# Kernel tuning notes

Measured on AMD Instinct MI355X. Metric: run time of the kernel, lower is better.

The kernel has to match this reference:

```python
import jax, jax.numpy as jnp
import numpy as np

B, T, K = 1024, 512, 64
START, STOP = K - 2, K - 1
NEG = -10000.0


def setup_inputs() -> dict:
    key = jax.random.key(0)
    k1, k2, k3, k4 = jax.random.split(key, 4)
    feats = jax.random.normal(k1, (B, T, K), dtype=jnp.float32)
    lengths = jax.random.randint(k2, (B,), 1, T + 1)  # valid seq lengths in [1, T]
    tags = jax.random.randint(k3, (B, T), 0, K)
    transitions = jax.random.normal(k4, (K, K), dtype=jnp.float32)
    # CRF constraints: nothing transitions INTO start, nothing transitions OUT of stop
    transitions = transitions.at[START, :].set(NEG).at[:, STOP].set(NEG)
    return {"feats": feats, "lengths": lengths, "tags": tags, "transitions": transitions}


def _forward_alg(feats, transitions, lengths):
    Bn, Tn, Kn = feats.shape
    alpha0 = jnp.full((Bn, Kn), NEG, feats.dtype).at[:, START].set(0.0)

    def step(alpha, emit):  # alpha: [B,K] over prev tag j; emit: [B,K] over cur tag i
        # tag_var[b,i,j] = emit[b,i] + trans[i,j] + alpha[b,j]
        new = jax.nn.logsumexp(emit[:, :, None] + transitions[None, :, :] + alpha[:, None, :], axis=2)
        return new, new

    _, ys = jax.lax.scan(step, alpha0, jnp.swapaxes(feats, 0, 1))  # ys: [T,B,K]
    all_alpha = jnp.concatenate([alpha0[None], ys], axis=0)  # [T+1,B,K]
    sel = all_alpha[lengths, jnp.arange(Bn)]  # alpha after `lengths` steps: [B,K]
    terminal = sel + transitions[STOP][None, :]
    return jax.nn.logsumexp(terminal, axis=1)  # [B]


def _score_sentence(feats, transitions, lengths, tags):
    Bn, Tn, Kn = feats.shape
    pad_start = jnp.concatenate([jnp.full((Bn, 1), START, tags.dtype), tags], axis=1)  # [B,T+1]
    pad_stop = jnp.concatenate([tags, jnp.full((Bn, 1), STOP, tags.dtype)], axis=1)  # [B,T+1]
    pos = jnp.arange(Tn + 1)[None, :]
    pad_stop = jnp.where(pos >= lengths[:, None], STOP, pad_stop)  # tags[lengths:] -> STOP
    trans_vals = transitions[pad_stop, pad_start]  # [B,T+1]
    trans_score = jnp.sum(jnp.where(pos <= lengths[:, None], trans_vals, 0.0), axis=1)
    emit_vals = jnp.take_along_axis(feats, tags[:, :, None], axis=2)[:, :, 0]  # [B,T]
    emit_mask = jnp.arange(Tn)[None, :] < lengths[:, None]
    emit_score = jnp.sum(jnp.where(emit_mask, emit_vals, 0.0), axis=1)
    return trans_score + emit_score


def reference(feats, lengths, tags, transitions):
    forward_score = _forward_alg(feats, transitions, lengths)
    gold_score = _score_sentence(feats, transitions, lengths, tags)
    return jnp.mean(forward_score - gold_score)
```

## Files before the change

kernel.cpp:

```cpp
#include <hip/hip_runtime.h>

#define CRF_B 1024
#define CRF_T 512
#define CRF_K 64
#define CRF_START 62
#define CRF_STOP 63

typedef float vf16 __attribute__((ext_vector_type(16)));

__device__ __forceinline__ float bcastf(float v, int lane) {
  return __int_as_float(__builtin_amdgcn_readlane(__float_as_int(v), lane));
}

__device__ __forceinline__ float wave_max64(float v) {
#pragma unroll
  for (int off = 32; off > 0; off >>= 1) v = fmaxf(v, __shfl_xor(v, off, 64));
  return v;
}

__device__ __forceinline__ float wave_sum64(float v) {
#pragma unroll
  for (int off = 32; off > 0; off >>= 1) v += __shfl_xor(v, off, 64);
  return v;
}

__global__ __launch_bounds__(128, 1) void crf_kernel(
    const float* __restrict__ feats, const int* __restrict__ lengths,
    const int* __restrict__ tags, const float* __restrict__ trans,
    float* __restrict__ out) {
  __shared__ float sT[CRF_K * 65];

  const int b = blockIdx.x;
  const int tid = threadIdx.x;
  const int lane = tid & 63;

  for (int idx = tid; idx < CRF_K * CRF_K; idx += 128)
    sT[(idx >> 6) * 65 + (idx & 63)] = trans[idx];
  __syncthreads();

  const int L = lengths[b];

  if (tid < 64) {
    vf16 E0, E1, E2, E3;
    {
      const float* trow = &sT[lane * 65];
#pragma unroll
      for (int j = 0; j < 16; ++j) E0[j] = __expf(trow[j]);
#pragma unroll
      for (int j = 0; j < 16; ++j) E1[j] = __expf(trow[16 + j]);
#pragma unroll
      for (int j = 0; j < 16; ++j) E2[j] = __expf(trow[32 + j]);
#pragma unroll
      for (int j = 0; j < 16; ++j) E3[j] = __expf(trow[48 + j]);
    }

    const float* bfeats = feats + (size_t)b * CRF_T * CRF_K + lane;

    float P = (lane == CRF_START) ? 1.0f : 0.0f;
    float offset = 0.0f;

    float e[8], f[8];
#pragma unroll
    for (int r = 0; r < 8; ++r) e[r] = bfeats[r * CRF_K];

    auto do_step = [&](float ee) {
      float a0 = 0.f, a1 = 0.f, a2 = 0.f, a3 = 0.f;
#pragma unroll
      for (int j = 0; j < 16; ++j) a0 = __builtin_fmaf(E0[j], bcastf(P, j), a0);
#pragma unroll
      for (int j = 0; j < 16; ++j) a1 = __builtin_fmaf(E1[j], bcastf(P, 16 + j), a1);
#pragma unroll
      for (int j = 0; j < 16; ++j) a2 = __builtin_fmaf(E2[j], bcastf(P, 32 + j), a2);
#pragma unroll
      for (int j = 0; j < 15; ++j) a3 = __builtin_fmaf(E3[j], bcastf(P, 48 + j), a3);
      P = ((a0 + a1) + (a2 + a3)) * ee;
    };

    auto rescale = [&](int first) {
      float M = first ? 1.0f : bcastf(P, 0);
      offset += __logf(M);
      P *= __builtin_amdgcn_rcpf(M);
    };

    const int Lb = L & ~7;
    for (int t0 = 0; t0 < Lb; t0 += 8) {
      const int tn = t0 + 8;
      if (tn < CRF_T) {
#pragma unroll
        for (int r = 0; r < 8; ++r) f[r] = bfeats[(tn + r) * CRF_K];
      } else {
#pragma unroll
        for (int r = 0; r < 8; ++r) f[r] = 0.0f;
      }
      float ee[8];
#pragma unroll
      for (int r = 0; r < 8; ++r) ee[r] = __expf(e[r]);

      rescale(t0 == 0);

#pragma unroll
      for (int r = 0; r < 8; ++r) do_step(ee[r]);
#pragma unroll
      for (int r = 0; r < 8; ++r) e[r] = f[r];
    }

    if (Lb < L) {
      rescale(Lb == 0);
#pragma unroll
      for (int r = 0; r < 8; ++r) {
        if (Lb + r < L) do_step(__expf(e[r]));
      }
    }

    float eST = __expf(sT[CRF_STOP * 65 + lane]);
    float v = P * eST;
    float s2 = wave_sum64(v);
    float fwd = offset + __logf(s2);
    if (lane == 0) atomicAdd(out, fwd * (1.0f / CRF_B));
  } else {
    const int* btags = tags + b * CRF_T;
    const float* bf = feats + (size_t)b * CRF_T * CRF_K;
    float gold = 0.0f;
#pragma unroll
    for (int base = 0; base < CRF_T; base += 64) {
      int t = base + lane;
      if (t < L) {
        int tg = btags[t];
        int tp = (t == 0) ? CRF_START : btags[t - 1];
        gold += bf[(size_t)t * CRF_K + tg];
        gold += sT[tg * 65 + tp];
      }
    }
    gold = wave_sum64(gold);
    if (lane == 0) {
      gold += sT[CRF_STOP * 65 + btags[L - 1]];
      atomicAdd(out, -gold * (1.0f / CRF_B));
    }
  }
}

extern "C" void kernel_launch(void* const* d_in, const int* in_sizes, int n_in,
                              void* d_out, int out_size, void* d_ws, size_t ws_size,
                              hipStream_t stream) {
  const float* feats = (const float*)d_in[0];
  const int* lengths = (const int*)d_in[1];
  const int* tags = (const int*)d_in[2];
  const float* trans = (const float*)d_in[3];
  float* out = (float*)d_out;
  hipMemsetAsync(out, 0, sizeof(float), stream);
  crf_kernel<<<CRF_B, 128, 0, stream>>>(feats, lengths, tags, trans, out);
}
```

Before: 299.7 us.

## Use packed fp16 dot2 for CRF forward recursion with per-step power-of-two rescaling

Each forward step's 64-wide dot product moves from fp32 FMAs with 63 readlane broadcasts to packed fp16 v_dot2 instructions on lane pairs. A DPP pair-swap packs two probabilities per lane, so only 32 readlanes are needed. Rescaling now happens every step, using a DPP wave-max and an exponent shift tracked as an integer offset, replacing the old per-8-step log/rcp rescale. This halves the broadcast and FMA count but adds a per-step max reduction and fp16 precision risk on exp(transitions) values, which can overflow or underflow fp16.

```diff
diff --git a/kernel.cpp b/kernel.cpp
--- a/kernel.cpp
+++ b/kernel.cpp
@@ -6,17 +6,23 @@
 #define CRF_START 62
 #define CRF_STOP 63
 
+typedef _Float16 hh2 __attribute__((ext_vector_type(2)));
+typedef unsigned int vu16 __attribute__((ext_vector_type(16)));
 typedef float vf16 __attribute__((ext_vector_type(16)));
+
+#if __has_builtin(__builtin_amdgcn_fdot2)
+#define USE_DOT2 1
+#else
+#define USE_DOT2 0
+#endif
 
 __device__ __forceinline__ float bcastf(float v, int lane) {
   return __int_as_float(__builtin_amdgcn_readlane(__float_as_int(v), lane));
 }
 
-__device__ __forceinline__ float wave_max64(float v) {
-#pragma unroll
-  for (int off = 32; off > 0; off >>= 1) v = fmaxf(v, __shfl_xor(v, off, 64));
-  return v;
-}
+#define DPP_F(x, ctrl, rmask)                                                 \
+  __int_as_float(__builtin_amdgcn_update_dpp(0, __float_as_int(x), ctrl,      \
+                                             rmask, 0xf, true))
 
 __device__ __forceinline__ float wave_sum64(float v) {
 #pragma unroll
@@ -41,45 +47,91 @@
   const int L = lengths[b];
 
   if (tid < 64) {
+    const float* trow = &sT[lane * 65];
+#if USE_DOT2
+    vu16 EA, EB;
+#pragma unroll
+    for (int jp = 0; jp < 16; ++jp) {
+      hh2 v;
+      v.x = (_Float16)__expf(trow[2 * jp]);
+      v.y = (_Float16)__expf(trow[2 * jp + 1]);
+      EA[jp] = __builtin_bit_cast(unsigned int, v);
+    }
+#pragma unroll
+    for (int jp = 0; jp < 16; ++jp) {
+      hh2 v;
+      v.x = (_Float16)__expf(trow[32 + 2 * jp]);
+      v.y = (_Float16)__expf(trow[32 + 2 * jp + 1]);
+      EB[jp] = __builtin_bit_cast(unsigned int, v);
+    }
+#else
     vf16 E0, E1, E2, E3;
-    {
-      const float* trow = &sT[lane * 65];
 #pragma unroll
-      for (int j = 0; j < 16; ++j) E0[j] = __expf(trow[j]);
+    for (int j = 0; j < 16; ++j) E0[j] = __expf(trow[j]);
 #pragma unroll
-      for (int j = 0; j < 16; ++j) E1[j] = __expf(trow[16 + j]);
+    for (int j = 0; j < 16; ++j) E1[j] = __expf(trow[16 + j]);
 #pragma unroll
-      for (int j = 0; j < 16; ++j) E2[j] = __expf(trow[32 + j]);
+    for (int j = 0; j < 16; ++j) E2[j] = __expf(trow[32 + j]);
 #pragma unroll
-      for (int j = 0; j < 16; ++j) E3[j] = __expf(trow[48 + j]);
-    }
+    for (int j = 0; j < 16; ++j) E3[j] = __expf(trow[48 + j]);
+#endif
 
     const float* bfeats = feats + (size_t)b * CRF_T * CRF_K + lane;
 
     float P = (lane == CRF_START) ? 1.0f : 0.0f;
-    float offset = 0.0f;
+    int offs = 0;
 
     float e[8], f[8];
 #pragma unroll
     for (int r = 0; r < 8; ++r) e[r] = bfeats[r * CRF_K];
 
     auto do_step = [&](float ee) {
+      float m = P;
+      m = fmaxf(m, DPP_F(m, 0x111, 0xf));
+      m = fmaxf(m, DPP_F(m, 0x112, 0xf));
+      m = fmaxf(m, DPP_F(m, 0x114, 0xf));
+      m = fmaxf(m, DPP_F(m, 0x118, 0xf));
+      m = fmaxf(m, DPP_F(m, 0x142, 0xa));
+      m = fmaxf(m, DPP_F(m, 0x143, 0xc));
+      float mx = bcastf(m, 63);
+      int ex = ((__float_as_int(mx) >> 23) & 0xff) - 126;
+      offs += ex;
+      float Pn = P * __int_as_float((127 - ex) << 23);
+#if USE_DOT2
+      _Float16 h = (_Float16)Pn;
+      int hi = (int)(unsigned short)__builtin_bit_cast(unsigned short, h);
+      int hn = __builtin_amdgcn_update_dpp(0, hi, 0xB1, 0xf, 0xf, true);
+      hh2 hp;
+      hp.x = h;
+      hp.y = __builtin_bit_cast(_Float16, (unsigned short)hn);
+      int hpi = __builtin_bit_cast(int, hp);
+      int rl[4];
+#pragma unroll
+      for (int q = 0; q < 4; ++q) rl[q] = __builtin_amdgcn_readlane(hpi, 2 * q);
       float a0 = 0.f, a1 = 0.f, a2 = 0.f, a3 = 0.f;
 #pragma unroll
-      for (int j = 0; j < 16; ++j) a0 = __builtin_fmaf(E0[j], bcastf(P, j), a0);
+      for (int jp = 0; jp < 32; ++jp) {
+        int cur = rl[jp & 3];
+        if (jp + 4 < 32)
+          rl[jp & 3] = __builtin_amdgcn_readlane(hpi, 2 * (jp + 4));
+        hh2 pb = __builtin_bit_cast(hh2, cur);
+        hh2 ev = __builtin_bit_cast(hh2, (jp < 16) ? EA[jp] : EB[jp - 16]);
+        float* acc = (jp & 3) == 0 ? &a0 : ((jp & 3) == 1 ? &a1 : ((jp & 3) == 2 ? &a2 : &a3));
+        *acc = __builtin_amdgcn_fdot2(ev, pb, *acc, false);
+      }
+      P = ((a0 + a1) + (a2 + a3)) * ee;
+#else
+      float a0 = 0.f, a1 = 0.f, a2 = 0.f, a3 = 0.f;
 #pragma unroll
-      for (int j = 0; j < 16; ++j) a1 = __builtin_fmaf(E1[j], bcastf(P, 16 + j), a1);
+      for (int j = 0; j < 16; ++j) a0 = __builtin_fmaf(E0[j], bcastf(Pn, j), a0);
 #pragma unroll
-      for (int j = 0; j < 16; ++j) a2 = __builtin_fmaf(E2[j], bcastf(P, 32 + j), a2);
+      for (int j = 0; j < 16; ++j) a1 = __builtin_fmaf(E1[j], bcastf(Pn, 16 + j), a1);
 #pragma unroll
-      for (int j = 0; j < 15; ++j) a3 = __builtin_fmaf(E3[j], bcastf(P, 48 + j), a3);
+      for (int j = 0; j < 16; ++j) a2 = __builtin_fmaf(E2[j], bcastf(Pn, 32 + j), a2);
+#pragma unroll
+      for (int j = 0; j < 15; ++j) a3 = __builtin_fmaf(E3[j], bcastf(Pn, 48 + j), a3);
       P = ((a0 + a1) + (a2 + a3)) * ee;
-    };
-
-    auto rescale = [&](int first) {
-      float M = first ? 1.0f : bcastf(P, 0);
-      offset += __logf(M);
-      P *= __builtin_amdgcn_rcpf(M);
+#endif
     };
 
     const int Lb = L & ~7;
@@ -95,27 +147,20 @@
       float ee[8];
 #pragma unroll
       for (int r = 0; r < 8; ++r) ee[r] = __expf(e[r]);
-
-      rescale(t0 == 0);
-
 #pragma unroll
       for (int r = 0; r < 8; ++r) do_step(ee[r]);
 #pragma unroll
       for (int r = 0; r < 8; ++r) e[r] = f[r];
     }
-
     if (Lb < L) {
-      rescale(Lb == 0);
 #pragma unroll
-      for (int r = 0; r < 8; ++r) {
+      for (int r = 0; r < 8; ++r)
         if (Lb + r < L) do_step(__expf(e[r]));
-      }
     }
 
     float eST = __expf(sT[CRF_STOP * 65 + lane]);
-    float v = P * eST;
-    float s2 = wave_sum64(v);
-    float fwd = offset + __logf(s2);
+    float s2 = wave_sum64(P * eST);
+    float fwd = (float)offs * 0.69314718056f + __logf(s2);
     if (lane == 0) atomicAdd(out, fwd * (1.0f / CRF_B));
   } else {
     const int* btags = tags + b * CRF_T;
```

New measurement: 307.6 us. 2.7% more time.
